# Performance work log

Measured on AMD Instinct MI355X. Metric: run time of the kernel, lower is better.

## Reference

```python
import jax, jax.numpy as jnp
import numpy as np

D, H, O, E, N = 1024, 2048, 1024, 8, 4096

def setup_inputs() -> dict:
    key = jax.random.key(0)
    ks = jax.random.split(key, 5)
    scale = lambda fan_in: 1.0 / np.sqrt(fan_in)
    x = jax.random.normal(ks[0], (N, D), dtype=jnp.float32)
    Wr = jax.random.normal(ks[1], (E, D), dtype=jnp.float32) * scale(D)
    br = jnp.zeros((E,), dtype=jnp.float32)
    W1 = jax.random.normal(ks[2], (E, H, D), dtype=jnp.float32) * scale(D)
    b1 = jnp.zeros((E, H), dtype=jnp.float32)
    W2 = jax.random.normal(ks[3], (E, O, H), dtype=jnp.float32) * scale(H)
    b2 = jnp.zeros((E, O), dtype=jnp.float32)
    return {"x": x, "Wr": Wr, "br": br, "W1": W1, "b1": b1, "W2": W2, "b2": b2}

def reference(x, Wr, br, W1, b1, W2, b2):
    # router softmax over experts: [N, E]
    route = jax.nn.softmax(x @ Wr.T + br, axis=-1)
    # all experts as one grouped GEMM: hidden [N, E, H]
    h = jnp.einsum('nd,ehd->neh', x, W1) + b1
    h = jnp.square(jax.nn.relu(h))  # squared ReLU
    # expert outputs [N, E, O]
    y = jnp.einsum('neh,eoh->neo', h, W2) + b2
    # softmax-weighted combine over experts -> [N, O]
    return jnp.einsum('ne,neo->no', route, y)
```

## Files before the change

### kernel.cpp

```cpp
#include <hip/hip_runtime.h>
#include <hip/hip_bf16.h>
#include <stdint.h>

#define Dd 1024
#define Hd 2048
#define Od 1024
#define Ed 8
#define Nd 4096

typedef __bf16 bf16x8 __attribute__((ext_vector_type(8)));
typedef float f32x4 __attribute__((ext_vector_type(4)));

__device__ __forceinline__ void gload16(const void* g, void* l) {
  __builtin_amdgcn_global_load_lds(
      (const __attribute__((address_space(1))) void*)g,
      (__attribute__((address_space(3))) void*)l, 16, 0, 0);
}

__device__ __forceinline__ unsigned short f2bf(float f) {
  __hip_bfloat16 h = __float2bfloat16(f);
  return *reinterpret_cast<unsigned short*>(&h);
}

__global__ void cvt_kernel(const float* __restrict__ in,
                           unsigned short* __restrict__ out, int ngroups) {
  int stride = gridDim.x * blockDim.x;
  for (int g = blockIdx.x * blockDim.x + threadIdx.x; g < ngroups; g += stride) {
    const float4* p = (const float4*)(in + (size_t)g * 8);
    float4 a = p[0], b = p[1];
    unsigned short o[8];
    o[0] = f2bf(a.x); o[1] = f2bf(a.y); o[2] = f2bf(a.z); o[3] = f2bf(a.w);
    o[4] = f2bf(b.x); o[5] = f2bf(b.y); o[6] = f2bf(b.z); o[7] = f2bf(b.w);
    *(int4*)(out + (size_t)g * 8) = *(int4*)o;
  }
}

__global__ void router_kernel(const float* __restrict__ x, const float* __restrict__ Wr,
                              const float* __restrict__ br, float* __restrict__ route,
                              unsigned short* __restrict__ xb) {
  const int n = blockIdx.x;
  const int t = threadIdx.x;
  __shared__ float xs[Dd];
  float4 v = *(const float4*)&x[(size_t)n * Dd + t * 4];
  *(float4*)&xs[t * 4] = v;
  unsigned short o[4] = {f2bf(v.x), f2bf(v.y), f2bf(v.z), f2bf(v.w)};
  *(uint2*)&xb[(size_t)n * Dd + t * 4] = *(const uint2*)o;
  __syncthreads();
  float p[Ed];
  #pragma unroll
  for (int e = 0; e < Ed; ++e) p[e] = 0.f;
  for (int d = t; d < Dd; d += 256) {
    float xv = xs[d];
    #pragma unroll
    for (int e = 0; e < Ed; ++e) p[e] += xv * Wr[e * Dd + d];
  }
  __shared__ float red[Ed][4];
  const int lane = t & 63, wid = t >> 6;
  #pragma unroll
  for (int e = 0; e < Ed; ++e) {
    float vv = p[e];
    for (int off = 32; off > 0; off >>= 1) vv += __shfl_down(vv, off);
    if (lane == 0) red[e][wid] = vv;
  }
  __syncthreads();
  if (t == 0) {
    float lg[Ed], mx = -1e30f;
    #pragma unroll
    for (int e = 0; e < Ed; ++e) {
      lg[e] = red[e][0] + red[e][1] + red[e][2] + red[e][3] + br[e];
      mx = fmaxf(mx, lg[e]);
    }
    float s = 0.f;
    #pragma unroll
    for (int e = 0; e < Ed; ++e) { lg[e] = expf(lg[e] - mx); s += lg[e]; }
    float inv = 1.f / s;
    #pragma unroll
    for (int e = 0; e < Ed; ++e) route[(size_t)n * Ed + e] = lg[e] * inv;
  }
}

__global__ void init_out_kernel(const float* __restrict__ route, const float* __restrict__ b2,
                                float* __restrict__ out) {
  const int idx = blockIdx.x * 256 + threadIdx.x;
  const int n = idx >> 10, o = idx & (Od - 1);
  float s = 0.f;
  #pragma unroll
  for (int e = 0; e < Ed; ++e) s += route[(size_t)n * Ed + e] * b2[e * Od + o];
  out[idx] = s;
}

template <int MODE>
__global__ __launch_bounds__(512, 2) void gemm8p(
    const unsigned short* __restrict__ Ag,
    const unsigned short* __restrict__ Bg,
    const float* __restrict__ bias,
    const float* __restrict__ route,
    void* __restrict__ Cout,
    int n0, int ncRows, int ngx) {
  extern __shared__ unsigned short smem[];
  unsigned short* As = smem;
  unsigned short* Bs = smem + 32768;

  const int nwg = gridDim.x;
  const int orig = blockIdx.x;
  const int q8 = nwg >> 3;
  const int wg = (orig & 7) * q8 + (orig >> 3);
  const int bx = wg % ngx;
  const int rem = wg / ngx;
  int by, ez;
  if (MODE == 0) { by = rem & 7; ez = rem >> 3; }
  else           { by = rem & 3; ez = rem >> 2; }

  const int tid = threadIdx.x;
  const int wid = tid >> 6, lane = tid & 63;
  const int wm = wid >> 2, wn = wid & 3;

  const int trow = tid >> 3;
  const int tcs = ((tid & 7) ^ (trow & 7)) * 8;

  const int NT = (MODE == 0) ? (Dd / 64) : (2 * Hd / 64);

  auto stageA = [&](int buf, int kt, int mh) {
    #pragma unroll
    for (int s = 0; s < 2; ++s) {
      const int pa = mh * 128 + s * 64 + trow;
      const int m = ((pa >> 6) & 1) * 128 + ((pa >> 7) & 1) * 64 + (pa & 63);
      const unsigned short* g;
      if (MODE == 0) {
        g = Ag + (size_t)(n0 + bx * 256 + m) * Dd + kt * 64 + tcs;
      } else {
        const int e = ez * 2 + (kt >> 5);
        g = Ag + (size_t)e * ncRows * Hd + (size_t)(bx * 256 + m) * Hd + (kt & 31) * 64 + tcs;
      }
      gload16(g, &As[(size_t)buf * 16384 + (size_t)(mh * 128 + s * 64) * 64 + wid * 512]);
    }
  };
  auto stageB = [&](int buf, int kt, int nh) {
    #pragma unroll
    for (int s = 0; s < 2; ++s) {
      const int pb = nh * 128 + s * 64 + trow;
      const int n = ((pb >> 5) & 3) * 64 + ((pb >> 7) & 1) * 32 + (pb & 31);
      const unsigned short* g;
      if (MODE == 0) {
        g = Bg + (size_t)ez * Hd * Dd + (size_t)(by * 256 + n) * Dd + kt * 64 + tcs;
      } else {
        const int e = ez * 2 + (kt >> 5);
        g = Bg + (size_t)e * Od * Hd + (size_t)(by * 256 + n) * Hd + (kt & 31) * 64 + tcs;
      }
      gload16(g, &Bs[(size_t)buf * 16384 + (size_t)(nh * 128 + s * 64) * 64 + wid * 512]);
    }
  };

  const int laneRow = lane & 15;
  const int swzc[2] = { ((lane >> 4) ^ (lane & 7)) << 3,
                        (((lane >> 4) + 4) ^ (lane & 7)) << 3 };
  const int aRowBase = (wm * 64 + laneRow) * 64;
  const int bRowBase = (wn * 32 + laneRow) * 64;

  auto rdA = [&](int buf, int mh, int mi, int kk) -> bf16x8 {
    const int addr = buf * 16384 + aRowBase + (mh * 128 + mi * 16) * 64 + swzc[kk];
    return *(const bf16x8*)&As[addr];
  };
  auto rdB = [&](int buf, int nh, int ni, int kk) -> bf16x8 {
    const int addr = buf * 16384 + bRowBase + (nh * 128 + ni * 16) * 64 + swzc[kk];
    return *(const bf16x8*)&Bs[addr];
  };

  f32x4 acc[8][4];
  #pragma unroll
  for (int i = 0; i < 8; ++i)
    #pragma unroll
    for (int j = 0; j < 4; ++j) acc[i][j] = (f32x4){0.f, 0.f, 0.f, 0.f};
  bf16x8 a0[4][2], a1[4][2], b0[2][2], b1[2][2];

  stageB(0, 0, 0); stageA(0, 0, 1); stageA(0, 0, 0); stageB(0, 0, 1);
  stageB(1, 1, 0); stageA(1, 1, 1);
  asm volatile("s_waitcnt vmcnt(4)" ::: "memory");
  __builtin_amdgcn_sched_barrier(0);
  __builtin_amdgcn_s_barrier();

  for (int U = 0; U < NT; ++U) {
    const int buf = U & 1, nbuf = buf ^ 1;
    #pragma unroll
    for (int mi = 0; mi < 4; ++mi) { a0[mi][0] = rdA(buf, 0, mi, 0); a0[mi][1] = rdA(buf, 0, mi, 1); }
    #pragma unroll
    for (int ni = 0; ni < 2; ++ni) { b0[ni][0] = rdB(buf, 0, ni, 0); b0[ni][1] = rdB(buf, 0, ni, 1); }
    if (U + 1 < NT) stageA(nbuf, U + 1, 0);
    __builtin_amdgcn_s_setprio(1);
    #pragma unroll
    for (int mi = 0; mi < 4; ++mi)
      #pragma unroll
      for (int ni = 0; ni < 2; ++ni) {
        acc[mi][ni] = __builtin_amdgcn_mfma_f32_16x16x32_bf16(a0[mi][0], b0[ni][0], acc[mi][ni], 0, 0, 0);
        acc[mi][ni] = __builtin_amdgcn_mfma_f32_16x16x32_bf16(a0[mi][1], b0[ni][1], acc[mi][ni], 0, 0, 0);
      }
    __builtin_amdgcn_s_setprio(0);
    __builtin_amdgcn_s_barrier();
    #pragma unroll
    for (int mi = 0; mi < 4; ++mi) { a1[mi][0] = rdA(buf, 1, mi, 0); a1[mi][1] = rdA(buf, 1, mi, 1); }
    if (U + 1 < NT) stageB(nbuf, U + 1, 1);
    __builtin_amdgcn_s_setprio(1);
    #pragma unroll
    for (int mi = 0; mi < 4; ++mi)
      #pragma unroll
      for (int ni = 0; ni < 2; ++ni) {
        acc[4 + mi][ni] = __builtin_amdgcn_mfma_f32_16x16x32_bf16(a1[mi][0], b0[ni][0], acc[4 + mi][ni], 0, 0, 0);
        acc[4 + mi][ni] = __builtin_amdgcn_mfma_f32_16x16x32_bf16(a1[mi][1], b0[ni][1], acc[4 + mi][ni], 0, 0, 0);
      }
    __builtin_amdgcn_s_setprio(0);
    __builtin_amdgcn_s_barrier();
    #pragma unroll
    for (int ni = 0; ni < 2; ++ni) { b1[ni][0] = rdB(buf, 1, ni, 0); b1[ni][1] = rdB(buf, 1, ni, 1); }
    if (U + 2 < NT) stageB(buf, U + 2, 0);
    __builtin_amdgcn_s_setprio(1);
    #pragma unroll
    for (int mi = 0; mi < 4; ++mi)
      #pragma unroll
      for (int ni = 0; ni < 2; ++ni) {
        acc[4 + mi][2 + ni] = __builtin_amdgcn_mfma_f32_16x16x32_bf16(a1[mi][0], b1[ni][0], acc[4 + mi][2 + ni], 0, 0, 0);
        acc[4 + mi][2 + ni] = __builtin_amdgcn_mfma_f32_16x16x32_bf16(a1[mi][1], b1[ni][1], acc[4 + mi][2 + ni], 0, 0, 0);
      }
    __builtin_amdgcn_s_setprio(0);
    __builtin_amdgcn_s_barrier();
    if (U + 2 < NT) stageA(buf, U + 2, 1);
    __builtin_amdgcn_s_setprio(1);
    #pragma unroll
    for (int mi = 0; mi < 4; ++mi)
      #pragma unroll
      for (int ni = 0; ni < 2; ++ni) {
        acc[mi][2 + ni] = __builtin_amdgcn_mfma_f32_16x16x32_bf16(a0[mi][0], b1[ni][0], acc[mi][2 + ni], 0, 0, 0);
        acc[mi][2 + ni] = __builtin_amdgcn_mfma_f32_16x16x32_bf16(a0[mi][1], b1[ni][1], acc[mi][2 + ni], 0, 0, 0);
      }
    __builtin_amdgcn_s_setprio(0);
    if (U + 2 < NT) {
      asm volatile("s_waitcnt vmcnt(4)" ::: "memory");
    } else if (U + 1 < NT) {
      asm volatile("s_waitcnt vmcnt(0)" ::: "memory");
    }
    __builtin_amdgcn_sched_barrier(0);
    __builtin_amdgcn_s_barrier();
  }

  if (MODE == 0) {
    unsigned short* hs = (unsigned short*)Cout;
    unsigned short* base = hs + (size_t)ez * ((size_t)ncRows * Hd);
    #pragma unroll
    for (int M = 0; M < 8; ++M) {
      const int mh = M >> 2, mi = M & 3;
      const int row = bx * 256 + wm * 128 + mh * 64 + mi * 16 + (lane >> 4) * 4;
      float rw[4];
      #pragma unroll
      for (int j = 0; j < 4; ++j) rw[j] = route[(size_t)(n0 + row + j) * Ed + ez];
      #pragma unroll
      for (int N = 0; N < 4; ++N) {
        const int nh = N >> 1, ni = N & 1;
        const int col = by * 256 + wn * 64 + nh * 32 + ni * 16 + (lane & 15);
        const float bv = bias[ez * Hd + col];
        #pragma unroll
        for (int j = 0; j < 4; ++j) {
          float v = acc[M][N][j] + bv;
          v = fmaxf(v, 0.f);
          v = v * v * rw[j];
          base[(size_t)(row + j) * Hd + col] = f2bf(v);
        }
      }
    }
  } else {
    float* out = (float*)Cout;
    #pragma unroll
    for (int M = 0; M < 8; ++M) {
      const int mh = M >> 2, mi = M & 3;
      const int row = n0 + bx * 256 + wm * 128 + mh * 64 + mi * 16 + (lane >> 4) * 4;
      #pragma unroll
      for (int N = 0; N < 4; ++N) {
        const int nh = N >> 1, ni = N & 1;
        const int col = by * 256 + wn * 64 + nh * 32 + ni * 16 + (lane & 15);
        #pragma unroll
        for (int j = 0; j < 4; ++j)
          atomicAdd(out + (size_t)(row + j) * Od + col, acc[M][N][j]);
      }
    }
  }
}

extern "C" void kernel_launch(void* const* d_in, const int* in_sizes, int n_in,
                              void* d_out, int out_size, void* d_ws, size_t ws_size,
                              hipStream_t stream) {
  const float* x  = (const float*)d_in[0];
  const float* Wr = (const float*)d_in[1];
  const float* br = (const float*)d_in[2];
  const float* W1 = (const float*)d_in[3];
  const float* b1 = (const float*)d_in[4];
  const float* W2 = (const float*)d_in[5];
  const float* b2 = (const float*)d_in[6];
  float* out = (float*)d_out;

  char* ws = (char*)d_ws;
  size_t off = 0;
  float* route = (float*)(ws + off);                 off += (size_t)Nd * Ed * 4;
  unsigned short* xb  = (unsigned short*)(ws + off); off += (size_t)Nd * Dd * 2;
  unsigned short* w1b = (unsigned short*)(ws + off); off += (size_t)Ed * Hd * Dd * 2;
  unsigned short* w2b = (unsigned short*)(ws + off); off += (size_t)Ed * Od * Hd * 2;
  unsigned short* hs  = (unsigned short*)(ws + off);

  size_t remain = (ws_size > off) ? (ws_size - off) : 0;
  const size_t perRow = (size_t)Ed * Hd * 2;
  long long ncMax = (long long)(remain / perRow);
  int NC = (int)(ncMax & ~255LL);
  if (NC > Nd) NC = Nd;
  if (NC < 256) NC = 256;

  hipFuncSetAttribute(reinterpret_cast<const void*>(&gemm8p<0>),
                      hipFuncAttributeMaxDynamicSharedMemorySize, 131072);
  hipFuncSetAttribute(reinterpret_cast<const void*>(&gemm8p<1>),
                      hipFuncAttributeMaxDynamicSharedMemorySize, 131072);

  cvt_kernel<<<2048, 256, 0, stream>>>(W1, w1b, Ed * Hd * Dd / 8);
  cvt_kernel<<<2048, 256, 0, stream>>>(W2, w2b, Ed * Od * Hd / 8);
  router_kernel<<<Nd, 256, 0, stream>>>(x, Wr, br, route, xb);
  init_out_kernel<<<Nd * Od / 256, 256, 0, stream>>>(route, b2, out);

  for (int n0 = 0; n0 < Nd; n0 += NC) {
    int nc = (NC < (Nd - n0)) ? NC : (Nd - n0);
    int ngx = nc / 256;
    gemm8p<0><<<ngx * 8 * Ed, 512, 131072, stream>>>(xb, w1b, b1, route, hs, n0, nc, ngx);
    gemm8p<1><<<ngx * 4 * 4, 512, 131072, stream>>>(hs, w2b, nullptr, nullptr, out, n0, nc, ngx);
  }
}
```

Before: 361.1 us.

## Simplify GEMM pipeline to plain double buffering with one barrier per tile

Replaces the staggered half-tile prefetch schedule, which staged pieces two tiles ahead with several intra-iteration barriers and partial vmcnt waits, with a simple double-buffer scheme. All four sub-tile loads for the next tile are issued at the top of each iteration, with a full vmcnt(0) wait and a single barrier at the end. The MFMA loops are reordered so the k-step is outermost, removing back-to-back dependent MFMAs on the same accumulator. This cuts barrier count but shortens the prefetch lead, so global-load latency may be less well hidden.

```diff
diff --git a/kernel.cpp b/kernel.cpp
--- a/kernel.cpp
+++ b/kernel.cpp
@@ -173,68 +173,62 @@
     for (int j = 0; j < 4; ++j) acc[i][j] = (f32x4){0.f, 0.f, 0.f, 0.f};
   bf16x8 a0[4][2], a1[4][2], b0[2][2], b1[2][2];
 
-  stageB(0, 0, 0); stageA(0, 0, 1); stageA(0, 0, 0); stageB(0, 0, 1);
-  stageB(1, 1, 0); stageA(1, 1, 1);
-  asm volatile("s_waitcnt vmcnt(4)" ::: "memory");
+  stageA(0, 0, 0); stageB(0, 0, 0); stageA(0, 0, 1); stageB(0, 0, 1);
+  asm volatile("s_waitcnt vmcnt(0)" ::: "memory");
   __builtin_amdgcn_sched_barrier(0);
   __builtin_amdgcn_s_barrier();
 
   for (int U = 0; U < NT; ++U) {
     const int buf = U & 1, nbuf = buf ^ 1;
+    if (U + 1 < NT) {
+      stageA(nbuf, U + 1, 0); stageB(nbuf, U + 1, 0);
+      stageA(nbuf, U + 1, 1); stageB(nbuf, U + 1, 1);
+    }
     #pragma unroll
     for (int mi = 0; mi < 4; ++mi) { a0[mi][0] = rdA(buf, 0, mi, 0); a0[mi][1] = rdA(buf, 0, mi, 1); }
     #pragma unroll
     for (int ni = 0; ni < 2; ++ni) { b0[ni][0] = rdB(buf, 0, ni, 0); b0[ni][1] = rdB(buf, 0, ni, 1); }
-    if (U + 1 < NT) stageA(nbuf, U + 1, 0);
     __builtin_amdgcn_s_setprio(1);
     #pragma unroll
-    for (int mi = 0; mi < 4; ++mi)
-      #pragma unroll
-      for (int ni = 0; ni < 2; ++ni) {
-        acc[mi][ni] = __builtin_amdgcn_mfma_f32_16x16x32_bf16(a0[mi][0], b0[ni][0], acc[mi][ni], 0, 0, 0);
-        acc[mi][ni] = __builtin_amdgcn_mfma_f32_16x16x32_bf16(a0[mi][1], b0[ni][1], acc[mi][ni], 0, 0, 0);
-      }
+    for (int kk = 0; kk < 2; ++kk)
+      #pragma unroll
+      for (int mi = 0; mi < 4; ++mi)
+        #pragma unroll
+        for (int ni = 0; ni < 2; ++ni)
+          acc[mi][ni] = __builtin_amdgcn_mfma_f32_16x16x32_bf16(a0[mi][kk], b0[ni][kk], acc[mi][ni], 0, 0, 0);
     __builtin_amdgcn_s_setprio(0);
-    __builtin_amdgcn_s_barrier();
     #pragma unroll
     for (int mi = 0; mi < 4; ++mi) { a1[mi][0] = rdA(buf, 1, mi, 0); a1[mi][1] = rdA(buf, 1, mi, 1); }
-    if (U + 1 < NT) stageB(nbuf, U + 1, 1);
     __builtin_amdgcn_s_setprio(1);
     #pragma unroll
-    for (int mi = 0; mi < 4; ++mi)
-      #pragma unroll
-      for (int ni = 0; ni < 2; ++ni) {
-        acc[4 + mi][ni] = __builtin_amdgcn_mfma_f32_16x16x32_bf16(a1[mi][0], b0[ni][0], acc[4 + mi][ni], 0, 0, 0);
-        acc[4 + mi][ni] = __builtin_amdgcn_mfma_f32_16x16x32_bf16(a1[mi][1], b0[ni][1], acc[4 + mi][ni], 0, 0, 0);
-      }
+    for (int kk = 0; kk < 2; ++kk)
+      #pragma unroll
+      for (int mi = 0; mi < 4; ++mi)
+        #pragma unroll
+        for (int ni = 0; ni < 2; ++ni)
+          acc[4 + mi][ni] = __builtin_amdgcn_mfma_f32_16x16x32_bf16(a1[mi][kk], b0[ni][kk], acc[4 + mi][ni], 0, 0, 0);
     __builtin_amdgcn_s_setprio(0);
-    __builtin_amdgcn_s_barrier();
     #pragma unroll
     for (int ni = 0; ni < 2; ++ni) { b1[ni][0] = rdB(buf, 1, ni, 0); b1[ni][1] = rdB(buf, 1, ni, 1); }
-    if (U + 2 < NT) stageB(buf, U + 2, 0);
     __builtin_amdgcn_s_setprio(1);
     #pragma unroll
-    for (int mi = 0; mi < 4; ++mi)
-      #pragma unroll
-      for (int ni = 0; ni < 2; ++ni) {
-        acc[4 + mi][2 + ni] = __builtin_amdgcn_mfma_f32_16x16x32_bf16(a1[mi][0], b1[ni][0], acc[4 + mi][2 + ni], 0, 0, 0);
-        acc[4 + mi][2 + ni] = __builtin_amdgcn_mfma_f32_16x16x32_bf16(a1[mi][1], b1[ni][1], acc[4 + mi][2 + ni], 0, 0, 0);
-      }
+    for (int kk = 0; kk < 2; ++kk)
+      #pragma unroll
+      for (int mi = 0; mi < 4; ++mi)
+        #pragma unroll
+        for (int ni = 0; ni < 2; ++ni)
+          acc[4 + mi][2 + ni] = __builtin_amdgcn_mfma_f32_16x16x32_bf16(a1[mi][kk], b1[ni][kk], acc[4 + mi][2 + ni], 0, 0, 0);
     __builtin_amdgcn_s_setprio(0);
-    __builtin_amdgcn_s_barrier();
-    if (U + 2 < NT) stageA(buf, U + 2, 1);
     __builtin_amdgcn_s_setprio(1);
     #pragma unroll
-    for (int mi = 0; mi < 4; ++mi)
-      #pragma unroll
-      for (int ni = 0; ni < 2; ++ni) {
-        acc[mi][2 + ni] = __builtin_amdgcn_mfma_f32_16x16x32_bf16(a0[mi][0], b1[ni][0], acc[mi][2 + ni], 0, 0, 0);
-        acc[mi][2 + ni] = __builtin_amdgcn_mfma_f32_16x16x32_bf16(a0[mi][1], b1[ni][1], acc[mi][2 + ni], 0, 0, 0);
-      }
+    for (int kk = 0; kk < 2; ++kk)
+      #pragma unroll
+      for (int mi = 0; mi < 4; ++mi)
+        #pragma unroll
+        for (int ni = 0; ni < 2; ++ni)
+          acc[mi][2 + ni] = __builtin_amdgcn_mfma_f32_16x16x32_bf16(a0[mi][kk], b1[ni][kk], acc[mi][2 + ni], 0, 0, 0);
     __builtin_amdgcn_s_setprio(0);
-    if (U + 2 < NT) {
-      asm volatile("s_waitcnt vmcnt(4)" ::: "memory");
-    } else if (U + 1 < NT) {
+    if (U + 1 < NT) {
       asm volatile("s_waitcnt vmcnt(0)" ::: "memory");
     }
     __builtin_amdgcn_sched_barrier(0);
```

Result: no change. 366.6 us (+1.5%).
